# Kernel optimization log

Hardware: AMD Instinct MI355X
Metric: run time of the kernel (lower is better)

## Reference

```python
import jax, jax.numpy as jnp
import numpy as np

SUPPORT = 1
NEIGHBOR = 20
STRIDE = 2
BS, V = 4, 2048


def _gather(feat, idx):
    # feat: (b, v, c), idx: (b, v, n) -> (b, v, n, c)
    b = feat.shape[0]
    return feat[jnp.arange(b)[:, None, None], idx]


def get_neighbor_index(vertices, k):
    # pairwise squared distances, take k nearest excluding self
    inner = jnp.einsum('bid,bjd->bij', vertices, vertices)
    sq = jnp.sum(vertices * vertices, axis=-1)
    dist = sq[:, :, None] - 2.0 * inner + sq[:, None, :]
    _, idx = jax.lax.top_k(-dist, k + 1)
    return idx[:, :, 1:]


def conv_layer(w, b, d, nbr, vertices, fmap, out_c):
    bs, v, n = nbr.shape
    diff = _gather(vertices, nbr) - vertices[:, :, None, :]  # (b,v,n,3)
    diff = diff / jnp.maximum(jnp.linalg.norm(diff, axis=-1, keepdims=True), 1e-12)
    dirn = d / jnp.maximum(jnp.linalg.norm(d, axis=0, keepdims=True), 1e-12)
    theta = jnp.einsum('bvnd,de->bvne', diff, dirn)  # (b,v,n,S*out)
    feat = fmap @ w + b  # (b,v,(S+1)*out)
    center = feat[..., :out_c]
    support = _gather(feat[..., out_c:], nbr)  # (b,v,n,S*out)
    act = (theta * support).reshape(bs, v, n, SUPPORT, out_c)
    act = jnp.sum(jnp.max(act, axis=2), axis=2)  # max over neighbors, sum over supports
    return center + act


LAYERS = [('c0', 3, 32), ('c1', 32, 64), ('c12', 64, 64), ('c13', 64, 64), ('c14', 64, 64),
          ('p1', 64, 64), ('c2', 64, 128), ('c3', 128, 256), ('c4', 256, 1024),
          ('c42', 1024, 1024), ('c43', 1024, 1024), ('c44', 1024, 1024)]


def _layer_params(key, in_c, out_c):
    k1, k2, k3 = jax.random.split(key, 3)
    stdv = 1.0 / np.sqrt((SUPPORT + 1) * out_c)
    w = jax.random.uniform(k1, (in_c, (SUPPORT + 1) * out_c), minval=-stdv, maxval=stdv, dtype=jnp.float32)
    b = jax.random.uniform(k2, ((SUPPORT + 1) * out_c,), minval=-stdv, maxval=stdv, dtype=jnp.float32)
    d = jax.random.uniform(k3, (3, SUPPORT * out_c), minval=-stdv, maxval=stdv, dtype=jnp.float32)
    return w, b, d


def setup_inputs() -> dict:
    key = jax.random.key(0)
    keys = jax.random.split(key, 20)
    inp = {'vertices': jax.random.normal(keys[0], (BS, V, 3), dtype=jnp.float32)}
    for i, (name, ic, oc) in enumerate(LAYERS):
        w, b, d = _layer_params(keys[i + 1], ic, oc)
        inp[name + '_w'], inp[name + '_b'], inp[name + '_d'] = w, b, d
    inp['fc1_w'] = jax.random.normal(keys[14], (1024, 256), dtype=jnp.float32) * 0.02
    inp['fc1_b'] = jnp.zeros((256,), jnp.float32)
    inp['bn_g'] = jnp.ones((256,), jnp.float32)
    inp['bn_b'] = jnp.zeros((256,), jnp.float32)
    inp['fc2_w'] = jax.random.normal(keys[15], (256, 40), dtype=jnp.float32) * 0.02
    inp['fc2_b'] = jnp.zeros((40,), jnp.float32)
    return inp


def reference(vertices, c0_w, c0_b, c0_d, c1_w, c1_b, c1_d, c12_w, c12_b, c12_d, c13_w, c13_b, c13_d, c14_w, c14_b, c14_d, p1_w, p1_b, p1_d, c2_w, c2_b, c2_d, c3_w, c3_b, c3_d, c4_w, c4_b, c4_d, c42_w, c42_b, c42_d, c43_w, c43_b, c43_d, c44_w, c44_b, c44_d, fc1_w, fc1_b, bn_g, bn_b, fc2_w, fc2_b):
    nbr = get_neighbor_index(vertices, NEIGHBOR)
    fm = conv_layer(c0_w, c0_b, c0_d, nbr, vertices, vertices, 32)
    fm = conv_layer(c1_w, c1_b, c1_d, nbr, vertices, fm, 64)
    fm = conv_layer(c12_w, c12_b, c12_d, nbr, vertices, fm, 64)
    fm = conv_layer(c13_w, c13_b, c13_d, nbr, vertices, fm, 64)
    fm = conv_layer(c14_w, c14_b, c14_d, nbr, vertices, fm, 64)
    # pool_1: conv, neighbor-max pooling, stride-2 vertex subsampling
    fm = conv_layer(p1_w, p1_b, p1_d, nbr, vertices, fm, 64)
    fm = jnp.max(_gather(fm, nbr), axis=2)
    sub = jnp.arange(0, vertices.shape[1], STRIDE)
    vertices2 = vertices[:, sub]
    fm = fm[:, sub]
    nbr2 = get_neighbor_index(vertices2, NEIGHBOR)
    fm = conv_layer(c2_w, c2_b, c2_d, nbr2, vertices2, fm, 128)
    fm = conv_layer(c3_w, c3_b, c3_d, nbr2, vertices2, fm, 256)
    fm = conv_layer(c4_w, c4_b, c4_d, nbr2, vertices2, fm, 1024)
    fm = conv_layer(c42_w, c42_b, c42_d, nbr2, vertices2, fm, 1024)
    fm = conv_layer(c43_w, c43_b, c43_d, nbr2, vertices2, fm, 1024)
    fm = conv_layer(c44_w, c44_b, c44_d, nbr2, vertices2, fm, 1024)
    g = jnp.max(fm, axis=1)  # (b, 1024) global max pool
    h = g @ fc1_w + fc1_b  # dropout = identity in eval
    h = h * jax.lax.rsqrt(jnp.float32(1.0 + 1e-5)) * bn_g + bn_b  # BN eval, running mean 0 / var 1
    h = jax.nn.relu(h)
    return h @ fc2_w + fc2_b
```

## Files before the change

kernel.cpp:

```cpp
#include <hip/hip_runtime.h>
#include <float.h>
#include <math.h>

#define BS 4
#define V1 2048
#define V2 1024
#define NB 20
#define KSEL 21

typedef __attribute__((ext_vector_type(8))) short short8v;
typedef __attribute__((ext_vector_type(4))) float f32x4;

__device__ __forceinline__ unsigned short f2bf(float x) {
    union { float f; unsigned u; } v; v.f = x;
    unsigned r = (v.u + 0x7fffu + ((v.u >> 16) & 1u)) >> 16;
    return (unsigned short)r;
}
__device__ __forceinline__ float bf2f(unsigned short h) {
    return __uint_as_float((unsigned)h << 16);
}
__device__ __forceinline__ unsigned umin32(unsigned a, unsigned b) { return a < b ? a : b; }

__device__ __forceinline__ void gload16(const void* g, void* l) {
    __builtin_amdgcn_global_load_lds((const __attribute__((address_space(1))) void*)g,
                                     (__attribute__((address_space(3))) void*)l, 16, 0, 0);
}

template<int SLOTS>
__global__ __launch_bounds__(256)
void knn_wave_kernel(const float* __restrict__ verts, int stride, int* __restrict__ nbr)
{
    constexpr int Vv = SLOTS * 64;
    __shared__ float xs[Vv], ys[Vv], zs[Vv];
    int tid = threadIdx.x;
    int lane = tid & 63;
    int wv = tid >> 6;
    int b = blockIdx.x / (Vv / 4);
    int q0 = (blockIdx.x % (Vv / 4)) * 4;
    const float* vb = verts + (size_t)b * V1 * 3;
    for (int p = tid; p < Vv; p += 256) {
        xs[p] = vb[(size_t)p * stride * 3 + 0];
        ys[p] = vb[(size_t)p * stride * 3 + 1];
        zs[p] = vb[(size_t)p * stride * 3 + 2];
    }
    __syncthreads();
    int i = q0 + wv;
    float xi = xs[i], yi = ys[i], zi = zs[i];
    float sqi = xi * xi + yi * yi + zi * zi;
    unsigned keys[SLOTS];
    #pragma unroll
    for (int s = 0; s < SLOTS; ++s) {
        int j = s * 64 + lane;
        float xj = xs[j], yj = ys[j], zj = zs[j];
        float sqj = xj * xj + yj * yj + zj * zj;
        float d = sqi - 2.0f * (xi * xj + yi * yj + zi * zj) + sqj;
        unsigned u = __float_as_uint(d);
        u = (u & 0x80000000u) ? ~u : (u | 0x80000000u);
        keys[s] = (u & ~31u) | (unsigned)s;
    }
    const unsigned UMAX = 0xFFFFFFFFu;
    unsigned c0 = UMAX, c1 = UMAX, c2 = UMAX, c3 = UMAX;
    #pragma unroll
    for (int s = 0; s < SLOTS; ++s) c0 = umin32(c0, keys[s]);
    #pragma unroll
    for (int s = 0; s < SLOTS; ++s) { unsigned k = keys[s]; if (k > c0) c1 = umin32(c1, k); }
    #pragma unroll
    for (int s = 0; s < SLOTS; ++s) { unsigned k = keys[s]; if (k > c1) c2 = umin32(c2, k); }
    #pragma unroll
    for (int s = 0; s < SLOTS; ++s) { unsigned k = keys[s]; if (k > c2) c3 = umin32(c3, k); }

    unsigned lm = c0;
    int* out = nbr + ((size_t)b * Vv + i) * NB;
    for (int it = 0; it < KSEL; ++it) {
        unsigned m = lm;
        #pragma unroll
        for (int off = 1; off < 64; off <<= 1)
            m = umin32(m, (unsigned)__shfl_xor((int)m, off));
        unsigned long long bal = __ballot(lm == m);
        int wl = __ffsll(bal) - 1;
        int slot = (int)(m & 31u);
        int j = slot * 64 + wl;
        if (it > 0 && lane == 0) out[it - 1] = j;
        if (lane == wl) {
            c0 = c1; c1 = c2; c2 = c3; c3 = UMAX;
            if (c0 == UMAX) {
                #pragma unroll
                for (int s = 0; s < SLOTS; ++s) {
                    unsigned k = keys[s];
                    if (k > m) c0 = umin32(c0, k);
                }
            }
            lm = c0;
        }
    }
}

__global__ __launch_bounds__(256)
void diffn_kernel(const float* __restrict__ verts, const int* __restrict__ nbr,
                  int Vv, int stride, float* __restrict__ diffn)
{
    int t = blockIdx.x * 256 + threadIdx.x;
    int total = BS * Vv * NB;
    if (t >= total) return;
    int v = (t / NB) % Vv;
    int b = t / (NB * Vv);
    const float* vb = verts + (size_t)b * V1 * 3;
    int j = nbr[t];
    float xi = vb[(size_t)v * stride * 3 + 0];
    float yi = vb[(size_t)v * stride * 3 + 1];
    float zi = vb[(size_t)v * stride * 3 + 2];
    float dx = vb[(size_t)j * stride * 3 + 0] - xi;
    float dy = vb[(size_t)j * stride * 3 + 1] - yi;
    float dz = vb[(size_t)j * stride * 3 + 2] - zi;
    float nrm = sqrtf(dx * dx + dy * dy + dz * dz);
    float inv = 1.0f / fmaxf(nrm, 1e-12f);
    diffn[(size_t)t * 3 + 0] = dx * inv;
    diffn[(size_t)t * 3 + 1] = dy * inv;
    diffn[(size_t)t * 3 + 2] = dz * inv;
}

struct ConvTArgs {
    const float* W[11];
    unsigned short* Wt[11];
    int K[11];
    int N[11];
    int tileoff[12];
};

__global__ __launch_bounds__(256)
void convT_all(ConvTArgs a)
{
    __shared__ float t[32][33];
    int g = blockIdx.x;
    int L = 0;
    #pragma unroll
    for (int q = 0; q < 10; ++q) if (g >= a.tileoff[q + 1]) L = q + 1;
    int rel = g - a.tileoff[L];
    int K = a.K[L], N = a.N[L];
    int tilesN = N >> 5;
    int k0 = (rel / tilesN) << 5, n0 = (rel % tilesN) << 5;
    const float* W = a.W[L];
    unsigned short* Wt = a.Wt[L];
    int tx = threadIdx.x & 31, ty = threadIdx.x >> 5;
    #pragma unroll
    for (int r = ty; r < 32; r += 8) t[r][tx] = W[(size_t)(k0 + r) * N + n0 + tx];
    __syncthreads();
    #pragma unroll
    for (int r = ty; r < 32; r += 8) Wt[(size_t)(n0 + r) * K + k0 + tx] = f2bf(t[tx][r]);
}

__global__ __launch_bounds__(256)
void c0_kernel(const float* __restrict__ verts, const float* __restrict__ W,
               const float* __restrict__ Bv, unsigned short* __restrict__ feat)
{
    int t = blockIdx.x * 256 + threadIdx.x;
    if (t >= BS * V1 * 64) return;
    int n = t & 63, m = t >> 6;
    float x = verts[(size_t)m * 3 + 0];
    float y = verts[(size_t)m * 3 + 1];
    float z = verts[(size_t)m * 3 + 2];
    feat[t] = f2bf(x * W[n] + y * W[64 + n] + z * W[128 + n] + Bv[n]);
}

template<int BK, int BM, int BN>
__global__ __launch_bounds__(256)
void gemm_mfma(const unsigned short* __restrict__ A, const unsigned short* __restrict__ Wt,
               const float* __restrict__ bias, unsigned short* __restrict__ C,
               int M, int N, int K)
{
    constexpr int RB = BK * 2;
    constexpr int TA = BM * RB;
    constexpr int TB = BN * RB;
    constexpr int SWM = (BK == 64) ? 7 : 3;
    constexpr int FI = BM / 32, FJ = BN / 32;
    constexpr int RA = TA / 4096, RBN = TB / 4096;
    constexpr int RMAX = (RA > RBN) ? RA : RBN;
    __shared__ __align__(16) char smem[TA + TB];
    int tid = threadIdx.x;
    int lane = tid & 63, wid = tid >> 6;
    int wr = wid >> 1, wc = wid & 1;

    int nwg = gridDim.x * gridDim.y;
    int orig = blockIdx.y * gridDim.x + blockIdx.x;
    int wg = orig;
    if ((nwg & 7) == 0) wg = (orig & 7) * (nwg >> 3) + (orig >> 3);
    int m0 = (wg / gridDim.x) * BM;
    int n0 = (wg % gridDim.x) * BN;

    f32x4 acc[FI][FJ] = {};

    int srow[RMAX], soffe[RMAX];
    #pragma unroll
    for (int r = 0; r < RMAX; ++r) {
        int L = r * 4096 + tid * 16;
        int row = L / RB;
        int off = (L % RB) ^ ((row & SWM) << 4);
        srow[r] = row; soffe[r] = off >> 1;
    }

    for (int kt = 0; kt < K; kt += BK) {
        #pragma unroll
        for (int r = 0; r < RA; ++r)
            gload16(A + (size_t)(m0 + srow[r]) * K + kt + soffe[r],
                    smem + r * 4096 + wid * 1024);
        #pragma unroll
        for (int r = 0; r < RBN; ++r)
            gload16(Wt + (size_t)(n0 + srow[r]) * K + kt + soffe[r],
                    smem + TA + r * 4096 + wid * 1024);
        asm volatile("s_waitcnt vmcnt(0)" ::: "memory");
        __syncthreads();
        #pragma unroll
        for (int ks = 0; ks < BK / 32; ++ks) {
            short8v av[FI], bv[FJ];
            #pragma unroll
            for (int i = 0; i < FI; ++i) {
                int row = wr * (BM / 2) + i * 16 + (lane & 15);
                int off = (ks * 64 + ((lane >> 4) * 16)) ^ ((row & SWM) << 4);
                av[i] = *(const short8v*)(smem + row * RB + off);
            }
            #pragma unroll
            for (int j = 0; j < FJ; ++j) {
                int row = wc * (BN / 2) + j * 16 + (lane & 15);
                int off = (ks * 64 + ((lane >> 4) * 16)) ^ ((row & SWM) << 4);
                bv[j] = *(const short8v*)(smem + TA + row * RB + off);
            }
            #pragma unroll
            for (int i = 0; i < FI; ++i)
                #pragma unroll
                for (int j = 0; j < FJ; ++j)
                    acc[i][j] = __builtin_amdgcn_mfma_f32_16x16x32_bf16(av[i], bv[j], acc[i][j], 0, 0, 0);
        }
        __syncthreads();
    }
    #pragma unroll
    for (int i = 0; i < FI; ++i) {
        #pragma unroll
        for (int j = 0; j < FJ; ++j) {
            int col = n0 + wc * (BN / 2) + j * 16 + (lane & 15);
            int rowb = m0 + wr * (BM / 2) + i * 16 + ((lane >> 4) * 4);
            float bv2 = bias[col];
            #pragma unroll
            for (int v = 0; v < 4; ++v)
                C[(size_t)(rowb + v) * N + col] = f2bf(acc[i][j][v] + bv2);
        }
    }
}

__global__ __launch_bounds__(256)
void act_kernel(const unsigned short* __restrict__ feat, const int* __restrict__ nbr,
                const float* __restrict__ diffn, const float* __restrict__ dmat,
                float* __restrict__ outp, unsigned short* __restrict__ outh,
                int Vv, int OC)
{
    int OC4 = OC >> 2;
    int t = blockIdx.x * 256 + threadIdx.x;
    int total = BS * Vv * OC4;
    if (t >= total) return;
    int c4 = t % OC4;
    int v = (t / OC4) % Vv;
    int b = t / (OC4 * Vv);
    const float4* d4 = (const float4*)dmat;
    float4 D0 = d4[c4], D1 = d4[OC4 + c4], D2 = d4[2 * OC4 + c4];
    float n0 = sqrtf(D0.x * D0.x + D1.x * D1.x + D2.x * D2.x);
    float n1 = sqrtf(D0.y * D0.y + D1.y * D1.y + D2.y * D2.y);
    float n2 = sqrtf(D0.z * D0.z + D1.z * D1.z + D2.z * D2.z);
    float n3 = sqrtf(D0.w * D0.w + D1.w * D1.w + D2.w * D2.w);
    float i0 = 1.0f / fmaxf(n0, 1e-12f);
    float i1 = 1.0f / fmaxf(n1, 1e-12f);
    float i2 = 1.0f / fmaxf(n2, 1e-12f);
    float i3 = 1.0f / fmaxf(n3, 1e-12f);
    D0.x *= i0; D0.y *= i1; D0.z *= i2; D0.w *= i3;
    D1.x *= i0; D1.y *= i1; D1.z *= i2; D1.w *= i3;
    D2.x *= i0; D2.y *= i1; D2.z *= i2; D2.w *= i3;

    const int* nb = nbr + ((size_t)b * Vv + v) * NB;
    const float* dfn = diffn + ((size_t)b * Vv + v) * NB * 3;
    const ushort4* frow = (const ushort4*)feat;
    size_t rowstride = (size_t)(2 * OC4);
    const ushort4* fsup = frow + (size_t)b * Vv * rowstride + OC4 + c4;
    float4 m = make_float4(-FLT_MAX, -FLT_MAX, -FLT_MAX, -FLT_MAX);
    for (int n = 0; n < NB; ++n) {
        int idx = nb[n];
        float e0 = dfn[3 * n + 0], e1 = dfn[3 * n + 1], e2 = dfn[3 * n + 2];
        ushort4 s = fsup[(size_t)idx * rowstride];
        float th;
        th = e0 * D0.x + e1 * D1.x + e2 * D2.x; m.x = fmaxf(m.x, th * bf2f(s.x));
        th = e0 * D0.y + e1 * D1.y + e2 * D2.y; m.y = fmaxf(m.y, th * bf2f(s.y));
        th = e0 * D0.z + e1 * D1.z + e2 * D2.z; m.z = fmaxf(m.z, th * bf2f(s.z));
        th = e0 * D0.w + e1 * D1.w + e2 * D2.w; m.w = fmaxf(m.w, th * bf2f(s.w));
    }
    ushort4 cen = frow[(size_t)b * Vv * rowstride + (size_t)v * rowstride + c4];
    float4 r = make_float4(bf2f(cen.x) + m.x, bf2f(cen.y) + m.y,
                           bf2f(cen.z) + m.z, bf2f(cen.w) + m.w);
    size_t oidx = ((size_t)b * Vv + v) * OC4 + c4;
    ushort4 h;
    h.x = f2bf(r.x); h.y = f2bf(r.y); h.z = f2bf(r.z); h.w = f2bf(r.w);
    ((ushort4*)outh)[oidx] = h;
    if (outp) ((float4*)outp)[oidx] = r;
}

__global__ __launch_bounds__(256)
void act1024_kernel(const unsigned short* __restrict__ feat, const int* __restrict__ nbr,
                    const float* __restrict__ diffn, const float* __restrict__ dmat,
                    float* __restrict__ outp, unsigned short* __restrict__ outh)
{
    const int OC4 = 256;
    int g = blockIdx.x;
    int b = (g & 7) >> 1;
    int v = ((g >> 3) << 1) | (g & 1);
    int c4 = threadIdx.x;
    const float4* d4 = (const float4*)dmat;
    float4 D0 = d4[c4], D1 = d4[OC4 + c4], D2 = d4[2 * OC4 + c4];
    float n0 = sqrtf(D0.x * D0.x + D1.x * D1.x + D2.x * D2.x);
    float n1 = sqrtf(D0.y * D0.y + D1.y * D1.y + D2.y * D2.y);
    float n2 = sqrtf(D0.z * D0.z + D1.z * D1.z + D2.z * D2.z);
    float n3 = sqrtf(D0.w * D0.w + D1.w * D1.w + D2.w * D2.w);
    float i0 = 1.0f / fmaxf(n0, 1e-12f);
    float i1 = 1.0f / fmaxf(n1, 1e-12f);
    float i2 = 1.0f / fmaxf(n2, 1e-12f);
    float i3 = 1.0f / fmaxf(n3, 1e-12f);
    D0.x *= i0; D0.y *= i1; D0.z *= i2; D0.w *= i3;
    D1.x *= i0; D1.y *= i1; D1.z *= i2; D1.w *= i3;
    D2.x *= i0; D2.y *= i1; D2.z *= i2; D2.w *= i3;

    const int* nb = nbr + ((size_t)b * V2 + v) * NB;
    const float* dfn = diffn + ((size_t)b * V2 + v) * NB * 3;
    const ushort4* frow = (const ushort4*)feat;
    const size_t rowstride = 2 * OC4;
    const ushort4* fsup = frow + (size_t)b * V2 * rowstride + OC4 + c4;
    float4 m = make_float4(-FLT_MAX, -FLT_MAX, -FLT_MAX, -FLT_MAX);
    for (int n = 0; n < NB; ++n) {
        int idx = nb[n];
        float e0 = dfn[3 * n + 0], e1 = dfn[3 * n + 1], e2 = dfn[3 * n + 2];
        ushort4 s = fsup[(size_t)idx * rowstride];
        float th;
        th = e0 * D0.x + e1 * D1.x + e2 * D2.x; m.x = fmaxf(m.x, th * bf2f(s.x));
        th = e0 * D0.y + e1 * D1.y + e2 * D2.y; m.y = fmaxf(m.y, th * bf2f(s.y));
        th = e0 * D0.z + e1 * D1.z + e2 * D2.z; m.z = fmaxf(m.z, th * bf2f(s.z));
        th = e0 * D0.w + e1 * D1.w + e2 * D2.w; m.w = fmaxf(m.w, th * bf2f(s.w));
    }
    ushort4 cen = frow[((size_t)b * V2 + v) * rowstride + c4];
    float4 r = make_float4(bf2f(cen.x) + m.x, bf2f(cen.y) + m.y,
                           bf2f(cen.z) + m.z, bf2f(cen.w) + m.w);
    size_t oidx = ((size_t)b * V2 + v) * OC4 + c4;
    ushort4 h;
    h.x = f2bf(r.x); h.y = f2bf(r.y); h.z = f2bf(r.z); h.w = f2bf(r.w);
    ((ushort4*)outh)[oidx] = h;
    if (outp) ((float4*)outp)[oidx] = r;
}

__global__ __launch_bounds__(256)
void pool_kernel(const ushort4* __restrict__ fmh, const int* __restrict__ nbr,
                 ushort4* __restrict__ outp)
{
    const int C4 = 16;
    int t = blockIdx.x * 256 + threadIdx.x;
    int total = BS * V2 * C4;
    if (t >= total) return;
    int c = t % C4;
    int v2 = (t / C4) % V2;
    int b = t / (C4 * V2);
    const int* nb = nbr + ((size_t)b * V1 + 2 * v2) * NB;
    float4 m = make_float4(-FLT_MAX, -FLT_MAX, -FLT_MAX, -FLT_MAX);
    for (int n = 0; n < NB; ++n) {
        int idx = nb[n];
        ushort4 s = fmh[((size_t)b * V1 + idx) * C4 + c];
        m.x = fmaxf(m.x, bf2f(s.x)); m.y = fmaxf(m.y, bf2f(s.y));
        m.z = fmaxf(m.z, bf2f(s.z)); m.w = fmaxf(m.w, bf2f(s.w));
    }
    ushort4 h;
    h.x = f2bf(m.x); h.y = f2bf(m.y); h.z = f2bf(m.z); h.w = f2bf(m.w);
    outp[((size_t)b * V2 + v2) * C4 + c] = h;
}

__global__ __launch_bounds__(256)
void gmax_part(const float* __restrict__ fm, float* __restrict__ part)
{
    int c = blockIdx.x * 256 + threadIdx.x;
    int ch = blockIdx.y;
    int b = blockIdx.z;
    float m = -FLT_MAX;
    for (int v = ch * 128; v < (ch + 1) * 128; ++v)
        m = fmaxf(m, fm[((size_t)b * V2 + v) * 1024 + c]);
    part[((size_t)b * 8 + ch) * 1024 + c] = m;
}

__global__ __launch_bounds__(256)
void gmax_final(const float* __restrict__ part, float* __restrict__ g)
{
    int t = blockIdx.x * 256 + threadIdx.x;
    if (t >= BS * 1024) return;
    int c = t % 1024, b = t / 1024;
    float m = -FLT_MAX;
    for (int ch = 0; ch < 8; ++ch)
        m = fmaxf(m, part[((size_t)b * 8 + ch) * 1024 + c]);
    g[t] = m;
}

__global__ __launch_bounds__(256)
void fc1_part(const float* __restrict__ g, const float* __restrict__ fc1w,
              float* __restrict__ hpart)
{
    int b = blockIdx.x, kg = blockIdx.y;
    int j = threadIdx.x;
    __shared__ float gs[128];
    if (j < 128) gs[j] = g[(size_t)b * 1024 + kg * 128 + j];
    __syncthreads();
    float h = 0.0f;
    #pragma unroll 4
    for (int k = 0; k < 128; ++k)
        h = fmaf(gs[k], fc1w[(size_t)(kg * 128 + k) * 256 + j], h);
    hpart[((size_t)b * 8 + kg) * 256 + j] = h;
}

__global__ __launch_bounds__(256)
void head2_kernel(const float* __restrict__ hpart, const float* __restrict__ fc1b,
                  const float* __restrict__ bng, const float* __restrict__ bnb,
                  const float* __restrict__ fc2w, const float* __restrict__ fc2b,
                  float* __restrict__ outp)
{
    __shared__ float hs[256];
    __shared__ float part[4][40];
    int b = blockIdx.x;
    int j = threadIdx.x;
    float s = fc1b[j];
    #pragma unroll
    for (int kg = 0; kg < 8; ++kg) s += hpart[((size_t)b * 8 + kg) * 256 + j];
    const float rc = 0.99999500003749937f;
    s = s * rc * bng[j] + bnb[j];
    hs[j] = fmaxf(s, 0.0f);
    __syncthreads();
    int ks = j >> 6, jo = j & 63;
    if (jo < 40) {
        float o = 0.0f;
        for (int k = ks * 64; k < ks * 64 + 64; ++k)
            o = fmaf(hs[k], fc2w[(size_t)k * 40 + jo], o);
        part[ks][jo] = o;
    }
    __syncthreads();
    if (j < 40)
        outp[(size_t)b * 40 + j] = fc2b[j] + part[0][j] + part[1][j] + part[2][j] + part[3][j];
}

extern "C" void kernel_launch(void* const* d_in, const int* in_sizes, int n_in,
                              void* d_out, int out_size, void* d_ws, size_t ws_size,
                              hipStream_t stream)
{
    (void)in_sizes; (void)n_in; (void)out_size; (void)ws_size;
    const float* verts = (const float*)d_in[0];
    auto Wp = [&](int i) { return (const float*)d_in[1 + 3 * i]; };
    auto Bp = [&](int i) { return (const float*)d_in[2 + 3 * i]; };
    auto Dp = [&](int i) { return (const float*)d_in[3 + 3 * i]; };
    const float* fc1w = (const float*)d_in[37];
    const float* fc1b = (const float*)d_in[38];
    const float* bng  = (const float*)d_in[39];
    const float* bnb  = (const float*)d_in[40];
    const float* fc2w = (const float*)d_in[41];
    const float* fc2b = (const float*)d_in[42];

    static const int IC[12] = {3, 32, 64, 64, 64, 64, 64, 128, 256, 1024, 1024, 1024};
    static const int OC[12] = {32, 64, 64, 64, 64, 64, 128, 256, 1024, 1024, 1024, 1024};

    char* ws = (char*)d_ws;
    size_t off = 0;
    auto alloc = [&](size_t bytes) {
        void* p = ws + off;
        off += (bytes + 255) & ~(size_t)255;
        return p;
    };
    int*   nbr1   = (int*)alloc((size_t)BS * V1 * NB * 4);
    int*   nbr2   = (int*)alloc((size_t)BS * V2 * NB * 4);
    float* diffn1 = (float*)alloc((size_t)BS * V1 * NB * 3 * 4);
    float* diffn2 = (float*)alloc((size_t)BS * V2 * NB * 3 * 4);
    unsigned short* feat = (unsigned short*)alloc((size_t)BS * V2 * 2048 * 2);
    unsigned short* fmh0 = (unsigned short*)alloc((size_t)BS * V2 * 1024 * 2);
    unsigned short* fmh1 = (unsigned short*)alloc((size_t)BS * V2 * 1024 * 2);
    float* fm32   = (float*)alloc((size_t)BS * V2 * 1024 * 4);
    float* gpart  = (float*)alloc((size_t)BS * 8 * 1024 * 4);
    float* g      = (float*)alloc((size_t)BS * 1024 * 4);
    float* hpart  = (float*)alloc((size_t)BS * 8 * 256 * 4);

    unsigned short* WtBuf[12];
    {
        size_t total = 0;
        for (int i = 1; i < 12; ++i) total += (size_t)(2 * OC[i]) * IC[i];
        unsigned short* base = (unsigned short*)alloc(total * 2);
        size_t o2 = 0;
        for (int i = 1; i < 12; ++i) { WtBuf[i] = base + o2; o2 += (size_t)(2 * OC[i]) * IC[i]; }
    }
    {
        ConvTArgs a;
        int toff = 0;
        for (int i = 1; i < 12; ++i) {
            int K = IC[i], N = 2 * OC[i];
            a.W[i - 1] = Wp(i);
            a.Wt[i - 1] = WtBuf[i];
            a.K[i - 1] = K;
            a.N[i - 1] = N;
            a.tileoff[i - 1] = toff;
            toff += (K / 32) * (N / 32);
        }
        a.tileoff[11] = toff;
        convT_all<<<toff, 256, 0, stream>>>(a);
    }

    auto gemm = [&](const unsigned short* A, int li, unsigned short* Cc, int M) {
        int K = IC[li], N = 2 * OC[li];
        if (N >= 1024) {
            dim3 gdim(N / 128, M / 128);
            gemm_mfma<64, 128, 128><<<gdim, 256, 0, stream>>>(A, WtBuf[li], Bp(li), Cc, M, N, K);
        } else if (K % 64 == 0) {
            dim3 gdim(N / 64, M / 64);
            gemm_mfma<64, 64, 64><<<gdim, 256, 0, stream>>>(A, WtBuf[li], Bp(li), Cc, M, N, K);
        } else {
            dim3 gdim(N / 64, M / 64);
            gemm_mfma<32, 64, 64><<<gdim, 256, 0, stream>>>(A, WtBuf[li], Bp(li), Cc, M, N, K);
        }
    };
    auto act = [&](const unsigned short* f, const int* nbr, const float* dfn, const float* d,
                   float* outp, unsigned short* outh, int Vv, int oc) {
        if (oc == 1024) {
            act1024_kernel<<<BS * V2, 256, 0, stream>>>(f, nbr, dfn, d, outp, outh);
        } else {
            int total = BS * Vv * (oc / 4);
            act_kernel<<<(total + 255) / 256, 256, 0, stream>>>(f, nbr, dfn, d, outp, outh, Vv, oc);
        }
    };

    knn_wave_kernel<32><<<BS * V1 / 4, 256, 0, stream>>>(verts, 1, nbr1);
    diffn_kernel<<<(BS * V1 * NB + 255) / 256, 256, 0, stream>>>(verts, nbr1, V1, 1, diffn1);

    c0_kernel<<<(BS * V1 * 64 + 255) / 256, 256, 0, stream>>>(verts, Wp(0), Bp(0), feat);
    unsigned short* hb[2] = {fmh0, fmh1};
    int pb = 0;
    act(feat, nbr1, diffn1, Dp(0), nullptr, hb[pb], V1, OC[0]);
    const unsigned short* cur = hb[pb]; pb ^= 1;

    for (int i = 1; i < 6; ++i) {
        gemm(cur, i, feat, BS * V1);
        act(feat, nbr1, diffn1, Dp(i), nullptr, hb[pb], V1, OC[i]);
        cur = hb[pb]; pb ^= 1;
    }

    {
        int total = BS * V2 * 16;
        pool_kernel<<<(total + 255) / 256, 256, 0, stream>>>(
            (const ushort4*)cur, nbr1, (ushort4*)hb[pb]);
        cur = hb[pb]; pb ^= 1;
    }

    knn_wave_kernel<16><<<BS * V2 / 4, 256, 0, stream>>>(verts, 2, nbr2);
    diffn_kernel<<<(BS * V2 * NB + 255) / 256, 256, 0, stream>>>(verts, nbr2, V2, 2, diffn2);

    for (int i = 6; i < 12; ++i) {
        gemm(cur, i, feat, BS * V2);
        float* f32out = (i == 11) ? fm32 : nullptr;
        act(feat, nbr2, diffn2, Dp(i), f32out, hb[pb], V2, OC[i]);
        cur = hb[pb]; pb ^= 1;
    }

    gmax_part<<<dim3(4, 8, BS), 256, 0, stream>>>(fm32, gpart);
    gmax_final<<<(BS * 1024 + 255) / 256, 256, 0, stream>>>(gpart, g);
    fc1_part<<<dim3(BS, 8), 256, 0, stream>>>(g, fc1w, hpart);
    head2_kernel<<<BS, 256, 0, stream>>>(hpart, fc1b, bng, bnb, fc2w, fc2b, (float*)d_out);
}
```

Measured before the change: 521.0 us.

## Fuse neighbor diff normalization into kNN and drop fp32 output path

The diffn computation moves into the kNN kernel: each lane keeps one selected neighbor index and writes it together with the normalized direction read from shared memory, so two diffn launches go away. The last layer no longer writes an fp32 copy, and the global max reads the bf16 activations instead. The gmax_final kernel is folded into fc1_part, which saves another launch. The risk is a small precision change, because the global max now runs on bf16-rounded values rather than fp32 ones.

```diff
diff --git a/kernel.cpp b/kernel.cpp
--- a/kernel.cpp
+++ b/kernel.cpp
@@ -28,7 +28,8 @@
 
 template<int SLOTS>
 __global__ __launch_bounds__(256)
-void knn_wave_kernel(const float* __restrict__ verts, int stride, int* __restrict__ nbr)
+void knn_wave_kernel(const float* __restrict__ verts, int stride, int* __restrict__ nbr,
+                     float* __restrict__ diffn)
 {
     constexpr int Vv = SLOTS * 64;
     __shared__ float xs[Vv], ys[Vv], zs[Vv];
@@ -70,7 +71,7 @@
     for (int s = 0; s < SLOTS; ++s) { unsigned k = keys[s]; if (k > c2) c3 = umin32(c3, k); }
 
     unsigned lm = c0;
-    int* out = nbr + ((size_t)b * Vv + i) * NB;
+    int myj = 0;
     for (int it = 0; it < KSEL; ++it) {
         unsigned m = lm;
         #pragma unroll
@@ -80,7 +81,7 @@
         int wl = __ffsll(bal) - 1;
         int slot = (int)(m & 31u);
         int j = slot * 64 + wl;
-        if (it > 0 && lane == 0) out[it - 1] = j;
+        if (lane == it - 1) myj = j;
         if (lane == wl) {
             c0 = c1; c1 = c2; c2 = c3; c3 = UMAX;
             if (c0 == UMAX) {
@@ -93,30 +94,14 @@
             lm = c0;
         }
     }
-}
-
-__global__ __launch_bounds__(256)
-void diffn_kernel(const float* __restrict__ verts, const int* __restrict__ nbr,
-                  int Vv, int stride, float* __restrict__ diffn)
-{
-    int t = blockIdx.x * 256 + threadIdx.x;
-    int total = BS * Vv * NB;
-    if (t >= total) return;
-    int v = (t / NB) % Vv;
-    int b = t / (NB * Vv);
-    const float* vb = verts + (size_t)b * V1 * 3;
-    int j = nbr[t];
-    float xi = vb[(size_t)v * stride * 3 + 0];
-    float yi = vb[(size_t)v * stride * 3 + 1];
-    float zi = vb[(size_t)v * stride * 3 + 2];
-    float dx = vb[(size_t)j * stride * 3 + 0] - xi;
-    float dy = vb[(size_t)j * stride * 3 + 1] - yi;
-    float dz = vb[(size_t)j * stride * 3 + 2] - zi;
-    float nrm = sqrtf(dx * dx + dy * dy + dz * dz);
-    float inv = 1.0f / fmaxf(nrm, 1e-12f);
-    diffn[(size_t)t * 3 + 0] = dx * inv;
-    diffn[(size_t)t * 3 + 1] = dy * inv;
-    diffn[(size_t)t * 3 + 2] = dz * inv;
+    if (lane < NB) {
+        nbr[((size_t)b * Vv + i) * NB + lane] = myj;
+        float dx = xs[myj] - xi, dy = ys[myj] - yi, dz = zs[myj] - zi;
+        float nrm = sqrtf(dx * dx + dy * dy + dz * dz);
+        float inv = 1.0f / fmaxf(nrm, 1e-12f);
+        float* dout = diffn + (((size_t)b * Vv + i) * NB + lane) * 3;
+        dout[0] = dx * inv; dout[1] = dy * inv; dout[2] = dz * inv;
+    }
 }
 
 struct ConvTArgs {
@@ -249,8 +234,7 @@
 __global__ __launch_bounds__(256)
 void act_kernel(const unsigned short* __restrict__ feat, const int* __restrict__ nbr,
                 const float* __restrict__ diffn, const float* __restrict__ dmat,
-                float* __restrict__ outp, unsigned short* __restrict__ outh,
-                int Vv, int OC)
+                unsigned short* __restrict__ outh, int Vv, int OC)
 {
     int OC4 = OC >> 2;
     int t = blockIdx.x * 256 + threadIdx.x;
@@ -290,19 +274,17 @@
         th = e0 * D0.w + e1 * D1.w + e2 * D2.w; m.w = fmaxf(m.w, th * bf2f(s.w));
     }
     ushort4 cen = frow[(size_t)b * Vv * rowstride + (size_t)v * rowstride + c4];
-    float4 r = make_float4(bf2f(cen.x) + m.x, bf2f(cen.y) + m.y,
-                           bf2f(cen.z) + m.z, bf2f(cen.w) + m.w);
     size_t oidx = ((size_t)b * Vv + v) * OC4 + c4;
     ushort4 h;
-    h.x = f2bf(r.x); h.y = f2bf(r.y); h.z = f2bf(r.z); h.w = f2bf(r.w);
+    h.x = f2bf(bf2f(cen.x) + m.x); h.y = f2bf(bf2f(cen.y) + m.y);
+    h.z = f2bf(bf2f(cen.z) + m.z); h.w = f2bf(bf2f(cen.w) + m.w);
     ((ushort4*)outh)[oidx] = h;
-    if (outp) ((float4*)outp)[oidx] = r;
 }
 
 __global__ __launch_bounds__(256)
 void act1024_kernel(const unsigned short* __restrict__ feat, const int* __restrict__ nbr,
                     const float* __restrict__ diffn, const float* __restrict__ dmat,
-                    float* __restrict__ outp, unsigned short* __restrict__ outh)
+                    unsigned short* __restrict__ outh)
 {
     const int OC4 = 256;
     int g = blockIdx.x;
@@ -340,13 +322,11 @@
         th = e0 * D0.w + e1 * D1.w + e2 * D2.w; m.w = fmaxf(m.w, th * bf2f(s.w));
     }
     ushort4 cen = frow[((size_t)b * V2 + v) * rowstride + c4];
-    float4 r = make_float4(bf2f(cen.x) + m.x, bf2f(cen.y) + m.y,
-                           bf2f(cen.z) + m.z, bf2f(cen.w) + m.w);
     size_t oidx = ((size_t)b * V2 + v) * OC4 + c4;
     ushort4 h;
-    h.x = f2bf(r.x); h.y = f2bf(r.y); h.z = f2bf(r.z); h.w = f2bf(r.w);
+    h.x = f2bf(bf2f(cen.x) + m.x); h.y = f2bf(bf2f(cen.y) + m.y);
+    h.z = f2bf(bf2f(cen.z) + m.z); h.w = f2bf(bf2f(cen.w) + m.w);
     ((ushort4*)outh)[oidx] = h;
-    if (outp) ((float4*)outp)[oidx] = r;
 }
 
 __global__ __launch_bounds__(256)
@@ -374,37 +354,31 @@
 }
 
 __global__ __launch_bounds__(256)
-void gmax_part(const float* __restrict__ fm, float* __restrict__ part)
+void gmax_part(const unsigned short* __restrict__ fm, float* __restrict__ part)
 {
     int c = blockIdx.x * 256 + threadIdx.x;
     int ch = blockIdx.y;
     int b = blockIdx.z;
     float m = -FLT_MAX;
     for (int v = ch * 128; v < (ch + 1) * 128; ++v)
-        m = fmaxf(m, fm[((size_t)b * V2 + v) * 1024 + c]);
+        m = fmaxf(m, bf2f(fm[((size_t)b * V2 + v) * 1024 + c]));
     part[((size_t)b * 8 + ch) * 1024 + c] = m;
 }
 
 __global__ __launch_bounds__(256)
-void gmax_final(const float* __restrict__ part, float* __restrict__ g)
-{
-    int t = blockIdx.x * 256 + threadIdx.x;
-    if (t >= BS * 1024) return;
-    int c = t % 1024, b = t / 1024;
-    float m = -FLT_MAX;
-    for (int ch = 0; ch < 8; ++ch)
-        m = fmaxf(m, part[((size_t)b * 8 + ch) * 1024 + c]);
-    g[t] = m;
-}
-
-__global__ __launch_bounds__(256)
-void fc1_part(const float* __restrict__ g, const float* __restrict__ fc1w,
+void fc1_part(const float* __restrict__ gpart, const float* __restrict__ fc1w,
               float* __restrict__ hpart)
 {
     int b = blockIdx.x, kg = blockIdx.y;
     int j = threadIdx.x;
     __shared__ float gs[128];
-    if (j < 128) gs[j] = g[(size_t)b * 1024 + kg * 128 + j];
+    if (j < 128) {
+        float m = -FLT_MAX;
+        #pragma unroll
+        for (int ch = 0; ch < 8; ++ch)
+            m = fmaxf(m, gpart[((size_t)b * 8 + ch) * 1024 + kg * 128 + j]);
+        gs[j] = m;
+    }
     __syncthreads();
     float h = 0.0f;
     #pragma unroll 4
@@ -475,9 +449,7 @@
     unsigned short* feat = (unsigned short*)alloc((size_t)BS * V2 * 2048 * 2);
     unsigned short* fmh0 = (unsigned short*)alloc((size_t)BS * V2 * 1024 * 2);
     unsigned short* fmh1 = (unsigned short*)alloc((size_t)BS * V2 * 1024 * 2);
-    float* fm32   = (float*)alloc((size_t)BS * V2 * 1024 * 4);
     float* gpart  = (float*)alloc((size_t)BS * 8 * 1024 * 4);
-    float* g      = (float*)alloc((size_t)BS * 1024 * 4);
     float* hpart  = (float*)alloc((size_t)BS * 8 * 256 * 4);
 
     unsigned short* WtBuf[12];
@@ -518,27 +490,27 @@
         }
     };
     auto act = [&](const unsigned short* f, const int* nbr, const float* dfn, const float* d,
-                   float* outp, unsigned short* outh, int Vv, int oc) {
+                   unsigned short* outh, int Vv, int oc) {
         if (oc == 1024) {
-            act1024_kernel<<<BS * V2, 256, 0, stream>>>(f, nbr, dfn, d, outp, outh);
+            act1024_kernel<<<BS * V2, 256, 0, stream>>>(f, nbr, dfn, d, outh);
         } else {
             int total = BS * Vv * (oc / 4);
-            act_kernel<<<(total + 255) / 256, 256, 0, stream>>>(f, nbr, dfn, d, outp, outh, Vv, oc);
+            act_kernel<<<(total + 255) / 256, 256, 0, stream>>>(f, nbr, dfn, d, outh, Vv, oc);
         }
     };
 
-    knn_wave_kernel<32><<<BS * V1 / 4, 256, 0, stream>>>(verts, 1, nbr1);
-    diffn_kernel<<<(BS * V1 * NB + 255) / 256, 256, 0, stream>>>(verts, nbr1, V1, 1, diffn1);
+    knn_wave_kernel<32><<<BS * V1 / 4, 256, 0, stream>>>(verts, 1, nbr1, diffn1);
+    knn_wave_kernel<16><<<BS * V2 / 4, 256, 0, stream>>>(verts, 2, nbr2, diffn2);
 
     c0_kernel<<<(BS * V1 * 64 + 255) / 256, 256, 0, stream>>>(verts, Wp(0), Bp(0), feat);
     unsigned short* hb[2] = {fmh0, fmh1};
     int pb = 0;
-    act(feat, nbr1, diffn1, Dp(0), nullptr, hb[pb], V1, OC[0]);
+    act(feat, nbr1, diffn1, Dp(0), hb[pb], V1, OC[0]);
     const unsigned short* cur = hb[pb]; pb ^= 1;
 
     for (int i = 1; i < 6; ++i) {
         gemm(cur, i, feat, BS * V1);
-        act(feat, nbr1, diffn1, Dp(i), nullptr, hb[pb], V1, OC[i]);
+        act(feat, nbr1, diffn1, Dp(i), hb[pb], V1, OC[i]);
         cur = hb[pb]; pb ^= 1;
     }
 
@@ -549,18 +521,13 @@
         cur = hb[pb]; pb ^= 1;
     }
 
-    knn_wave_kernel<16><<<BS * V2 / 4, 256, 0, stream>>>(verts, 2, nbr2);
-    diffn_kernel<<<(BS * V2 * NB + 255) / 256, 256, 0, stream>>>(verts, nbr2, V2, 2, diffn2);
-
     for (int i = 6; i < 12; ++i) {
         gemm(cur, i, feat, BS * V2);
-        float* f32out = (i == 11) ? fm32 : nullptr;
-        act(feat, nbr2, diffn2, Dp(i), f32out, hb[pb], V2, OC[i]);
+        act(feat, nbr2, diffn2, Dp(i), hb[pb], V2, OC[i]);
         cur = hb[pb]; pb ^= 1;
     }
 
-    gmax_part<<<dim3(4, 8, BS), 256, 0, stream>>>(fm32, gpart);
-    gmax_final<<<(BS * 1024 + 255) / 256, 256, 0, stream>>>(gpart, g);
-    fc1_part<<<dim3(BS, 8), 256, 0, stream>>>(g, fc1w, hpart);
+    gmax_part<<<dim3(4, 8, BS), 256, 0, stream>>>(cur, gpart);
+    fc1_part<<<dim3(BS, 8), 256, 0, stream>>>(gpart, fc1w, hpart);
     head2_kernel<<<BS, 256, 0, stream>>>(hpart, fc1b, bng, bnb, fc2w, fc2b, (float*)d_out);
 }
```

Result: no change. 516.3 us (-0.9%).
